# Performance work log

Hardware: AMD Instinct MI355X
Metric: run time of the kernel (lower is better)

## Reference

```python
import jax, jax.numpy as jnp
import numpy as np

C = 128
K = 23
D = 3
ALPHA = 0.5
K_D = max(1, K // D)          # 7
S = 2 * D - 1                 # 5
C4 = C // 4 if C >= 4 else 1  # 32


def dwconv(x, w, pad, dil):
    # x: [B,C,H,W], w: [C,1,kh,kw] depthwise (groups=C)
    return jax.lax.conv_general_dilated(
        x, w, window_strides=(1, 1), padding=pad, rhs_dilation=dil,
        dimension_numbers=('NCHW', 'OIHW', 'NCHW'),
        feature_group_count=x.shape[1])


def setup_inputs() -> dict:
    key = jax.random.key(0)
    ks = jax.random.split(key, 10)
    sc = 0.1
    return {
        'x': jax.random.normal(ks[0], (4, C, 256, 256), jnp.float32),
        'h1_w': jax.random.normal(ks[1], (C, 1, 1, S), jnp.float32) * sc,
        'h2_w': jax.random.normal(ks[2], (C, 1, 1, K_D), jnp.float32) * sc,
        'v1_w': jax.random.normal(ks[3], (C, 1, S, 1), jnp.float32) * sc,
        'v2_w': jax.random.normal(ks[4], (C, 1, K_D, 1), jnp.float32) * sc,
        'g1_w': jax.random.normal(ks[5], (C4, 2 * C), jnp.float32) * sc,
        'g2_w': jax.random.normal(ks[6], (2, C4), jnp.float32) * sc,
        'g2_b': jnp.zeros((2,), jnp.float32),
        'fuse_w': jax.random.normal(ks[7], (C, C), jnp.float32) * sc,
        'fuse_b': jnp.zeros((C,), jnp.float32),
    }


def reference(x, h1_w, h2_w, v1_w, v2_w, g1_w, g2_w, g2_b, fuse_w, fuse_b):
    # directional depthwise large-kernel paths
    h = dwconv(x, h1_w, [(0, 0), (S // 2, S // 2)], (1, 1))
    h = dwconv(h, h2_w, [(0, 0), ((K_D - 1) * D // 2, (K_D - 1) * D // 2)], (1, D))
    v = dwconv(x, v1_w, [(S // 2, S // 2), (0, 0)], (1, 1))
    v = dwconv(v, v2_w, [((K_D - 1) * D // 2, (K_D - 1) * D // 2), (0, 0)], (D, 1))
    # gate: global avg pool over concat[h, v] -> 1x1 MLP -> softmax over 2 dirs
    pooled = jnp.concatenate([h.mean(axis=(2, 3)), v.mean(axis=(2, 3))], axis=1)  # [B, 2C]
    g = pooled @ g1_w.T
    g = g * jax.nn.sigmoid(g)  # SiLU
    w = jax.nn.softmax(g @ g2_w.T + g2_b, axis=1)  # [B, 2]
    wh = w[:, 0][:, None, None, None]
    wv = w[:, 1][:, None, None, None]
    attn = wh * h + wv * v
    # 1x1 fuse conv
    attn = jnp.einsum('bchw,oc->bohw', attn, fuse_w) + fuse_b[None, :, None, None]
    y = x * attn
    return x + ALPHA * (y - x)
```

## Files before the change

kernel.cpp:

```cpp
#include <hip/hip_runtime.h>
#include <hip/hip_bf16.h>

#define CCH 128
#define HGT 256
#define WID 256
#define HW  65536

typedef __attribute__((ext_vector_type(8))) short short8;
typedef __attribute__((ext_vector_type(4))) float floatx4;


__device__ __forceinline__ float bf2f(unsigned short u) {
  return __uint_as_float(((unsigned)u) << 16);
}
__device__ __forceinline__ short f2bfs(float f) {
  return (short)__bfloat16_as_ushort(__float2bfloat16(f));
}

__global__ __launch_bounds__(256) void prep_kernel(float* __restrict__ sums) {
  int t = threadIdx.x;
  for (int i = t; i < 1032; i += 256) sums[i] = 0.f;
}

__global__ __launch_bounds__(256) void conv_kernel(
    const float* __restrict__ x,
    const float* __restrict__ h1w, const float* __restrict__ h2w,
    const float* __restrict__ v1w, const float* __restrict__ v2w,
    __hip_bfloat16* __restrict__ hbuf, __hip_bfloat16* __restrict__ vbuf,
    float* __restrict__ sum_h, float* __restrict__ sum_v) {
  int d = blockIdx.x;
  int l = (d & 7) * 1536 + (d >> 3);
  int t = threadIdx.x;
  float acc = 0.f;
  int bcg;
  float* sums;
  if (l < 8192) {
    int bc = l >> 4;
    int c = bc & (CCH - 1);
    int row = (l & 15) * 16 + (t >> 4);
    int p0 = (t & 15) * 16;
    const float* xr = x + (size_t)bc * HW + (size_t)row * WID;
    float w1[5], w2[7];
#pragma unroll
    for (int i = 0; i < 5; ++i) w1[i] = h1w[c * 5 + i];
#pragma unroll
    for (int j = 0; j < 7; ++j) w2[j] = h2w[c * 7 + j];
    float xv[40];
#pragma unroll
    for (int k = 0; k < 10; ++k) {
      int col = p0 - 12 + 4 * k;
      float4 v = make_float4(0.f, 0.f, 0.f, 0.f);
      if (col >= 0 && col < WID) v = *(const float4*)(xr + col);
      xv[4 * k] = v.x; xv[4 * k + 1] = v.y; xv[4 * k + 2] = v.z; xv[4 * k + 3] = v.w;
    }
    float s1[34];
#pragma unroll
    for (int m = 0; m < 34; ++m) {
      int q = p0 - 9 + m;
      float s = 0.f;
#pragma unroll
      for (int i = 0; i < 5; ++i) s = fmaf(xv[m + 1 + i], w1[i], s);
      s1[m] = ((unsigned)q < (unsigned)WID) ? s : 0.f;
    }
    short8 st0, st1;
#pragma unroll
    for (int u = 0; u < 16; ++u) {
      float s = 0.f;
#pragma unroll
      for (int j = 0; j < 7; ++j) s = fmaf(s1[u + 3 * j], w2[j], s);
      if (u < 8) st0[u] = f2bfs(s); else st1[u - 8] = f2bfs(s);
      acc += s;
    }
    unsigned short* hp = (unsigned short*)hbuf + (size_t)bc * HW + (size_t)row * WID + p0;
    *(short8*)hp = st0;
    *(short8*)(hp + 8) = st1;
    bcg = bc; sums = sum_h;
  } else {
    int lb = l - 8192;
    int bc = lb >> 3;
    int c = bc & (CCH - 1);
    int y0 = (lb & 7) * 32;
    const float* xc = x + (size_t)bc * HW + t;
    float w1[5], w2[7];
#pragma unroll
    for (int i = 0; i < 5; ++i) w1[i] = v1w[c * 5 + i];
#pragma unroll
    for (int j = 0; j < 7; ++j) w2[j] = v2w[c * 7 + j];
    float xv[54];
#pragma unroll
    for (int m = 0; m < 54; ++m) {
      int yy = y0 - 11 + m;
      xv[m] = ((unsigned)yy < (unsigned)HGT) ? xc[(size_t)yy * WID] : 0.f;
    }
    float s1[50];
#pragma unroll
    for (int m = 0; m < 50; ++m) {
      int q = y0 - 9 + m;
      float s = 0.f;
#pragma unroll
      for (int i = 0; i < 5; ++i) s = fmaf(xv[m + i], w1[i], s);
      s1[m] = ((unsigned)q < (unsigned)HGT) ? s : 0.f;
    }
    unsigned short* vp = (unsigned short*)vbuf + (size_t)bc * HW + t;
#pragma unroll
    for (int u = 0; u < 32; ++u) {
      float s = 0.f;
#pragma unroll
      for (int j = 0; j < 7; ++j) s = fmaf(s1[u + 3 * j], w2[j], s);
      vp[(size_t)(y0 + u) * WID] = (unsigned short)f2bfs(s);
      acc += s;
    }
    bcg = bc; sums = sum_v;
  }
#pragma unroll
  for (int off = 32; off > 0; off >>= 1) acc += __shfl_down(acc, off);
  if ((t & 63) == 0) atomicAdd(&sums[bcg], acc);
}

__global__ __launch_bounds__(128) void gate_kernel(
    const float* __restrict__ sum_h, const float* __restrict__ sum_v,
    const float* __restrict__ g1w, const float* __restrict__ g2w,
    const float* __restrict__ g2b, float* __restrict__ wgate) {
  int t = threadIdx.x;
  __shared__ float gs[4][32];
  int b = t >> 5, r = t & 31;
  {
    float acc = 0.f;
    const float inv = 1.f / 65536.f;
    for (int k = 0; k < 128; ++k)
      acc = fmaf(sum_h[b * 128 + k] * inv, g1w[r * 256 + k], acc);
    for (int k = 0; k < 128; ++k)
      acc = fmaf(sum_v[b * 128 + k] * inv, g1w[r * 256 + 128 + k], acc);
    float sig = 1.f / (1.f + expf(-acc));
    gs[b][r] = acc * sig;
  }
  __syncthreads();
  if (t < 4) {
    float t0 = g2b[0], t1 = g2b[1];
    for (int rr = 0; rr < 32; ++rr) {
      t0 = fmaf(gs[t][rr], g2w[rr], t0);
      t1 = fmaf(gs[t][rr], g2w[32 + rr], t1);
    }
    float mx = fmaxf(t0, t1);
    float e0 = expf(t0 - mx), e1 = expf(t1 - mx);
    float inv = 1.f / (e0 + e1);
    wgate[t * 2 + 0] = e0 * inv;
    wgate[t * 2 + 1] = e1 * inv;
  }
}

__global__ __launch_bounds__(256, 4) void fuse_kernel(
    const float* __restrict__ x, const __hip_bfloat16* __restrict__ hbuf,
    const __hip_bfloat16* __restrict__ vbuf, const float* __restrict__ fuse_w,
    const float* __restrict__ fuse_b, const float* __restrict__ wgate,
    float* __restrict__ out) {
  __shared__ unsigned short aT[128 * 128];
  int bid = blockIdx.x;
  int half = bid & 1;
  int y = (bid >> 1) & 255;
  int b = bid >> 9;
  int t = threadIdx.x;
  int w = t >> 6, lane = t & 63;
  int quad = lane >> 4, n16 = lane & 15;
  float wh = wgate[b * 2], wv = wgate[b * 2 + 1];

  size_t base = (size_t)(b * CCH) * HW + (size_t)y * WID + half * 128;
  const unsigned short* hb = (const unsigned short*)hbuf;
  const unsigned short* vb = (const unsigned short*)vbuf;
  int cth = t >> 4;
  int p0 = (t & 15) * 8;

  short8 hv[16];
#pragma unroll
  for (int cpass = 0; cpass < 8; ++cpass) {
    int c = cpass * 16 + cth;
    size_t gi = base + (size_t)c * HW + p0;
    hv[2 * cpass]     = *(const short8*)(hb + gi);
    hv[2 * cpass + 1] = *(const short8*)(vb + gi);
  }
#pragma unroll
  for (int cpass = 0; cpass < 8; ++cpass) {
    int c = cpass * 16 + cth;
    int g = c >> 3, c7 = c & 7;
#pragma unroll
    for (int e = 0; e < 8; ++e) {
      float a = fmaf(wh, bf2f((unsigned short)hv[2 * cpass][e]),
                     wv * bf2f((unsigned short)hv[2 * cpass + 1][e]));
      int p = p0 + e;
      int gp = g ^ (p & 15) ^ (p >> 4);
      aT[p * 128 + gp * 8 + c7] = (unsigned short)f2bfs(a);
    }
  }

  short8 wf[2][4];
#pragma unroll
  for (int ni = 0; ni < 2; ++ni) {
    int o = (2 * w + ni) * 16 + n16;
#pragma unroll
    for (int kt = 0; kt < 4; ++kt) {
      const float* wp = fuse_w + o * 128 + kt * 32 + quad * 8;
      float4 f0 = *(const float4*)wp;
      float4 f1 = *(const float4*)(wp + 4);
      short8 s;
      s[0] = f2bfs(f0.x); s[1] = f2bfs(f0.y); s[2] = f2bfs(f0.z); s[3] = f2bfs(f0.w);
      s[4] = f2bfs(f1.x); s[5] = f2bfs(f1.y); s[6] = f2bfs(f1.z); s[7] = f2bfs(f1.w);
      wf[ni][kt] = s;
    }
  }
  __syncthreads();

  floatx4 acc[8][2];
#pragma unroll
  for (int mt = 0; mt < 8; ++mt)
#pragma unroll
    for (int ni = 0; ni < 2; ++ni) acc[mt][ni] = (floatx4)0.f;

#pragma unroll
  for (int kt = 0; kt < 4; ++kt) {
#pragma unroll
    for (int mt = 0; mt < 8; ++mt) {
      int p = mt * 16 + n16;
      int gp = (4 * kt + quad) ^ (p & 15) ^ (p >> 4);
      short8 afr = *(const short8*)&aT[p * 128 + gp * 8];
      acc[mt][0] = __builtin_amdgcn_mfma_f32_16x16x32_bf16(afr, wf[0][kt], acc[mt][0], 0, 0, 0);
      acc[mt][1] = __builtin_amdgcn_mfma_f32_16x16x32_bf16(afr, wf[1][kt], acc[mt][1], 0, 0, 0);
    }
  }

  float fb0 = fuse_b[(2 * w) * 16 + n16];
  float fb1 = fuse_b[(2 * w + 1) * 16 + n16];
  size_t ob0 = base + (size_t)((2 * w) * 16 + n16) * HW;
  size_t ob1 = base + (size_t)((2 * w + 1) * 16 + n16) * HW;
#pragma unroll
  for (int mt = 0; mt < 8; ++mt) {
    int pq = mt * 16 + quad * 4;
    float4 x0 = *(const float4*)(x + ob0 + pq);
    float4 x1 = *(const float4*)(x + ob1 + pq);
    floatx4 a0 = acc[mt][0], a1 = acc[mt][1];
    float4 r0, r1;
    r0.x = x0.x * fmaf(0.5f, fb0 + a0[0], 0.5f);
    r0.y = x0.y * fmaf(0.5f, fb0 + a0[1], 0.5f);
    r0.z = x0.z * fmaf(0.5f, fb0 + a0[2], 0.5f);
    r0.w = x0.w * fmaf(0.5f, fb0 + a0[3], 0.5f);
    r1.x = x1.x * fmaf(0.5f, fb1 + a1[0], 0.5f);
    r1.y = x1.y * fmaf(0.5f, fb1 + a1[1], 0.5f);
    r1.z = x1.z * fmaf(0.5f, fb1 + a1[2], 0.5f);
    r1.w = x1.w * fmaf(0.5f, fb1 + a1[3], 0.5f);
    *(float4*)(out + ob0 + pq) = r0;
    *(float4*)(out + ob1 + pq) = r1;
  }
}

extern "C" void kernel_launch(void* const* d_in, const int* in_sizes, int n_in,
                              void* d_out, int out_size, void* d_ws, size_t ws_size,
                              hipStream_t stream) {
  const float* x      = (const float*)d_in[0];
  const float* h1w    = (const float*)d_in[1];
  const float* h2w    = (const float*)d_in[2];
  const float* v1w    = (const float*)d_in[3];
  const float* v2w    = (const float*)d_in[4];
  const float* g1w    = (const float*)d_in[5];
  const float* g2w    = (const float*)d_in[6];
  const float* g2b    = (const float*)d_in[7];
  const float* fusew  = (const float*)d_in[8];
  const float* fuseb  = (const float*)d_in[9];
  float* out = (float*)d_out;

  float* sums  = (float*)d_ws;
  float* sum_h = sums;
  float* sum_v = sums + 512;
  float* wgate = sums + 1024;
  __hip_bfloat16* hbuf = (__hip_bfloat16*)((char*)d_ws + 32768);
  __hip_bfloat16* vbuf = hbuf + (size_t)4 * CCH * HW;

  prep_kernel<<<1, 256, 0, stream>>>(sums);
  conv_kernel<<<12288, 256, 0, stream>>>(x, h1w, h2w, v1w, v2w, hbuf, vbuf, sum_h, sum_v);
  gate_kernel<<<1, 128, 0, stream>>>(sum_h, sum_v, g1w, g2w, g2b, wgate);
  fuse_kernel<<<4 * HGT * 2, 256, 0, stream>>>(x, hbuf, vbuf, fusew, fuseb, wgate, out);
}
```

Baseline: 386.8 us.

## Retile vertical conv to 2 columns × 8 rows per thread, memset sums

```diff
diff --git a/kernel.cpp b/kernel.cpp
--- a/kernel.cpp
+++ b/kernel.cpp
@@ -17,19 +17,14 @@
   return (short)__bfloat16_as_ushort(__float2bfloat16(f));
 }
 
-__global__ __launch_bounds__(256) void prep_kernel(float* __restrict__ sums) {
-  int t = threadIdx.x;
-  for (int i = t; i < 1032; i += 256) sums[i] = 0.f;
-}
-
-__global__ __launch_bounds__(256) void conv_kernel(
+__global__ __launch_bounds__(256, 4) void conv_kernel(
     const float* __restrict__ x,
     const float* __restrict__ h1w, const float* __restrict__ h2w,
     const float* __restrict__ v1w, const float* __restrict__ v2w,
     __hip_bfloat16* __restrict__ hbuf, __hip_bfloat16* __restrict__ vbuf,
     float* __restrict__ sum_h, float* __restrict__ sum_v) {
   int d = blockIdx.x;
-  int l = (d & 7) * 1536 + (d >> 3);
+  int l = (d & 7) * 2048 + (d >> 3);
   int t = threadIdx.x;
   float acc = 0.f;
   int bcg;
@@ -77,39 +72,52 @@
     bcg = bc; sums = sum_h;
   } else {
     int lb = l - 8192;
-    int bc = lb >> 3;
+    int bc = lb >> 4;
     int c = bc & (CCH - 1);
-    int y0 = (lb & 7) * 32;
-    const float* xc = x + (size_t)bc * HW + t;
+    int cp = (t & 127) * 2;
+    int y0 = (lb & 15) * 16 + (t >> 7) * 8;
+    const float* xc = x + (size_t)bc * HW + cp;
     float w1[5], w2[7];
 #pragma unroll
     for (int i = 0; i < 5; ++i) w1[i] = v1w[c * 5 + i];
 #pragma unroll
     for (int j = 0; j < 7; ++j) w2[j] = v2w[c * 7 + j];
-    float xv[54];
-#pragma unroll
-    for (int m = 0; m < 54; ++m) {
+    float2 xq[30];
+#pragma unroll
+    for (int m = 0; m < 30; ++m) {
       int yy = y0 - 11 + m;
-      xv[m] = ((unsigned)yy < (unsigned)HGT) ? xc[(size_t)yy * WID] : 0.f;
-    }
-    float s1[50];
-#pragma unroll
-    for (int m = 0; m < 50; ++m) {
-      int q = y0 - 9 + m;
-      float s = 0.f;
-#pragma unroll
-      for (int i = 0; i < 5; ++i) s = fmaf(xv[m + i], w1[i], s);
-      s1[m] = ((unsigned)q < (unsigned)HGT) ? s : 0.f;
-    }
-    unsigned short* vp = (unsigned short*)vbuf + (size_t)bc * HW + t;
-#pragma unroll
-    for (int u = 0; u < 32; ++u) {
-      float s = 0.f;
-#pragma unroll
-      for (int j = 0; j < 7; ++j) s = fmaf(s1[u + 3 * j], w2[j], s);
-      vp[(size_t)(y0 + u) * WID] = (unsigned short)f2bfs(s);
-      acc += s;
-    }
+      xq[m] = ((unsigned)yy < (unsigned)HGT) ? *(const float2*)(xc + (size_t)yy * WID)
+                                             : make_float2(0.f, 0.f);
+    }
+    ushort2 res[8];
+#pragma unroll
+    for (int cc = 0; cc < 2; ++cc) {
+      float s1[26];
+#pragma unroll
+      for (int m = 0; m < 26; ++m) {
+        int q = y0 - 9 + m;
+        float s = 0.f;
+#pragma unroll
+        for (int i = 0; i < 5; ++i) {
+          float xv = (cc == 0) ? xq[m + i].x : xq[m + i].y;
+          s = fmaf(xv, w1[i], s);
+        }
+        s1[m] = ((unsigned)q < (unsigned)HGT) ? s : 0.f;
+      }
+#pragma unroll
+      for (int u = 0; u < 8; ++u) {
+        float s = 0.f;
+#pragma unroll
+        for (int j = 0; j < 7; ++j) s = fmaf(s1[u + 3 * j], w2[j], s);
+        unsigned short bs = (unsigned short)f2bfs(s);
+        if (cc == 0) res[u].x = bs; else res[u].y = bs;
+        acc += s;
+      }
+    }
+    unsigned short* vp = (unsigned short*)vbuf + (size_t)bc * HW + cp;
+#pragma unroll
+    for (int u = 0; u < 8; ++u)
+      *(ushort2*)(vp + (size_t)(y0 + u) * WID) = res[u];
     bcg = bc; sums = sum_v;
   }
 #pragma unroll
@@ -273,8 +281,8 @@
   __hip_bfloat16* hbuf = (__hip_bfloat16*)((char*)d_ws + 32768);
   __hip_bfloat16* vbuf = hbuf + (size_t)4 * CCH * HW;
 
-  prep_kernel<<<1, 256, 0, stream>>>(sums);
-  conv_kernel<<<12288, 256, 0, stream>>>(x, h1w, h2w, v1w, v2w, hbuf, vbuf, sum_h, sum_v);
+  hipMemsetAsync(d_ws, 0, 1032 * sizeof(float), stream);
+  conv_kernel<<<16384, 256, 0, stream>>>(x, h1w, h2w, v1w, v2w, hbuf, vbuf, sum_h, sum_v);
   gate_kernel<<<1, 128, 0, stream>>>(sum_h, sum_v, g1w, g2w, g2b, wgate);
   fuse_kernel<<<4 * HGT * 2, 256, 0, stream>>>(x, hbuf, vbuf, fusew, fuseb, wgate, out);
 }
```

After: 401.6 us. 1.04x slower.
